# Kernel tuning notes

Measured on AMD Instinct MI355X. Metric: run time of the kernel, lower is better.

## Reference

```python
import jax, jax.numpy as jnp
import numpy as np


def setup_inputs() -> dict:
    key = jax.random.key(0)
    ks = jax.random.split(key, 7)
    B, C, W, H = 4, 256, 128, 128
    s = 1.0 / np.sqrt(C)
    return {
        "x": jax.random.normal(ks[0], (B, C, W, H), dtype=jnp.float32),
        "wq": jax.random.normal(ks[1], (C, C), dtype=jnp.float32) * s,
        "bq": jax.random.normal(ks[2], (C,), dtype=jnp.float32) * s,
        "wk": jax.random.normal(ks[3], (C, C), dtype=jnp.float32) * s,
        "bk": jax.random.normal(ks[4], (C,), dtype=jnp.float32) * s,
        "wv": jax.random.normal(ks[5], (C, C), dtype=jnp.float32) * s,
        "bv": jax.random.normal(ks[6], (C,), dtype=jnp.float32) * s,
    }


def reference(x, wq, bq, wk, bk, wv, bv):
    B, C, W, H = x.shape
    N = W * H
    xf = x.reshape(B, C, N)  # flatten spatial: (B, C, N)
    # 1x1 convs are channel-mixing GEMMs: out[b,o,n] = sum_c w[o,c] x[b,c,n] + b[o]
    q = jnp.einsum('oc,bcn->bon', wq, xf) + bq[:, None]
    k = jnp.einsum('oc,bcn->bon', wk, xf) + bk[:, None]
    v = jnp.einsum('oc,bcn->bon', wv, xf) + bv[:, None]
    # channel-channel energy: (B, C, C)
    energy = jnp.einsum('bcn,bdn->bcd', q, k) / jnp.sqrt(jnp.float32(N))
    attention = jax.nn.softmax(energy, axis=-1)
    out = jnp.einsum('bcd,bdn->bcn', attention, v)
    return out.reshape(B, C, W, H) + x
```

## Files before the change

### kernel.cpp

```cpp
#include <hip/hip_runtime.h>
#include <stdint.h>

#define BB 4
#define CC 256
#define NN 16384
#define NSL 32

typedef unsigned short u16;
typedef __attribute__((ext_vector_type(8))) __bf16 bf16x8;
typedef __attribute__((ext_vector_type(4))) float f32x4;

__device__ __forceinline__ u16 f2bf(float f) {
  union { float f; uint32_t u; } c;
  c.f = f;
  uint32_t u = c.u;
  return (u16)((u + 0x7fffu + ((u >> 16) & 1u)) >> 16);
}

__device__ __forceinline__ void g2l16(const u16* g, u16* l) {
  __builtin_amdgcn_global_load_lds((__attribute__((address_space(1))) void*)g,
                                   (__attribute__((address_space(3))) void*)l, 16, 0, 0);
}

__device__ __forceinline__ void stage256x32_w8(const u16* src, int stride, u16* lds, int tid) {
  int r = tid >> 2;
  int c = (tid & 3) << 3;
  g2l16(src + (size_t)r * stride + c, lds + r * 32 + c);
  g2l16(src + (size_t)(r + 128) * stride + c, lds + (r + 128) * 32 + c);
}

__device__ __forceinline__ void mfma_tile(const u16* As, const u16* Bs, int mb, int nb,
                                          int l16, int q8, f32x4 acc[4][4]) {
  bf16x8 af[4], bf[4];
#pragma unroll
  for (int i = 0; i < 4; i++) af[i] = *(const bf16x8*)&As[(mb + i * 16 + l16) * 32 + q8];
#pragma unroll
  for (int i = 0; i < 4; i++) bf[i] = *(const bf16x8*)&Bs[(nb + i * 16 + l16) * 32 + q8];
#pragma unroll
  for (int i = 0; i < 4; i++)
#pragma unroll
    for (int j = 0; j < 4; j++)
      acc[i][j] = __builtin_amdgcn_mfma_f32_16x16x32_bf16(af[i], bf[j], acc[i][j], 0, 0, 0);
}

__device__ __forceinline__ void mfma_tile48(const u16* As, const u16* Bs, int mb, int nb,
                                            int l16, int q8, f32x4 acc[4][8]) {
  bf16x8 af[4], bf[8];
#pragma unroll
  for (int i = 0; i < 4; i++) af[i] = *(const bf16x8*)&As[(mb + i * 16 + l16) * 32 + q8];
#pragma unroll
  for (int j = 0; j < 8; j++) bf[j] = *(const bf16x8*)&Bs[(nb + j * 16 + l16) * 32 + q8];
#pragma unroll
  for (int i = 0; i < 4; i++)
#pragma unroll
    for (int j = 0; j < 8; j++)
      acc[i][j] = __builtin_amdgcn_mfma_f32_16x16x32_bf16(af[i], bf[j], acc[i][j], 0, 0, 0);
}

__global__ __launch_bounds__(256) void prep_kernel(const float* __restrict__ x,
                                                   u16* __restrict__ xb,
                                                   u16* __restrict__ xbT,
                                                   float* __restrict__ s_part) {
  __shared__ float t[64][65];
  __shared__ float rs[64][4];
  int n0 = blockIdx.x * 64, c0 = blockIdx.y * 64, bz = blockIdx.z;
  int tid = threadIdx.x;
  int rr0 = tid >> 4, q4 = (tid & 15) * 4;
  const float* xs = x + ((size_t)bz * CC + c0) * NN + n0;
  u16* xbp = xb + ((size_t)bz * CC + c0) * NN + n0;
#pragma unroll
  for (int cc = rr0; cc < 64; cc += 16) {
    float4 v = *(const float4*)&xs[(size_t)cc * NN + q4];
    t[cc][q4] = v.x; t[cc][q4 + 1] = v.y; t[cc][q4 + 2] = v.z; t[cc][q4 + 3] = v.w;
    union { u16 h[4]; uint2 u; } pk;
    pk.h[0] = f2bf(v.x); pk.h[1] = f2bf(v.y); pk.h[2] = f2bf(v.z); pk.h[3] = f2bf(v.w);
    *(uint2*)&xbp[(size_t)cc * NN + q4] = pk.u;
  }
  __syncthreads();
  {
    int r = tid >> 2, q = tid & 3;
    float p = 0.f;
#pragma unroll
    for (int i = 0; i < 16; i++) p += t[r][q * 16 + i];
    rs[r][q] = p;
  }
  u16* od = xbT + ((size_t)bz * NN + n0) * CC + c0;
#pragma unroll
  for (int nn = rr0; nn < 64; nn += 16) {
    union { u16 h[4]; uint2 u; } pk;
    pk.h[0] = f2bf(t[q4][nn]); pk.h[1] = f2bf(t[q4 + 1][nn]);
    pk.h[2] = f2bf(t[q4 + 2][nn]); pk.h[3] = f2bf(t[q4 + 3][nn]);
    *(uint2*)&od[(size_t)nn * CC + q4] = pk.u;
  }
  __syncthreads();
  if (tid < 64)
    s_part[((size_t)bz * 256 + blockIdx.x) * CC + c0 + tid] =
        rs[tid][0] + rs[tid][1] + rs[tid][2] + rs[tid][3];
}

__global__ __launch_bounds__(512) void gram_kernel(const u16* __restrict__ xb,
                                                   float* __restrict__ Gp) {
  __shared__ u16 As[2][256 * 32];
  int tid = threadIdx.x;
  int d0 = blockIdx.x * 128;
  int sl = blockIdx.y, bz = blockIdx.z;
  const u16* A = xb + (size_t)bz * CC * NN + sl * 512;
  f32x4 acc[4][4] = {};
  int wave = tid >> 6, lane = tid & 63;
  int mb = (wave & 3) * 64, nb = d0 + (wave >> 2) * 64;
  int quad = lane >> 4, l16 = lane & 15, q8 = quad * 8;
  for (int kk = 0; kk < 512; kk += 64) {
    stage256x32_w8(A + kk, NN, As[0], tid);
    stage256x32_w8(A + kk + 32, NN, As[1], tid);
    __syncthreads();
    mfma_tile(As[0], As[0], mb, nb, l16, q8, acc);
    mfma_tile(As[1], As[1], mb, nb, l16, q8, acc);
    __syncthreads();
  }
  float* gp = Gp + ((size_t)sl * BB + bz) * CC * CC;
#pragma unroll
  for (int i = 0; i < 4; i++)
#pragma unroll
    for (int j = 0; j < 4; j++)
#pragma unroll
      for (int r = 0; r < 4; r++)
        gp[(size_t)(mb + i * 16 + quad * 4 + r) * CC + nb + j * 16 + l16] =
            acc[i][j][r];
}

__global__ __launch_bounds__(256) void reduce_kernel(const float* __restrict__ Gp,
                                                     const float* __restrict__ s_part,
                                                     const float* __restrict__ Wk,
                                                     float* __restrict__ G,
                                                     float* __restrict__ s,
                                                     float* __restrict__ WkT) {
  __shared__ float tw[32][33];
  int t = threadIdx.x, blk = blockIdx.x;
  size_t base = ((size_t)blk * 256 + t) * 4;
  float ax = 0.f, ay = 0.f, az = 0.f, aw = 0.f;
#pragma unroll 8
  for (int sl = 0; sl < NSL; sl++) {
    float4 v = *(const float4*)&Gp[(size_t)sl * (BB * CC * CC) + base];
    ax += v.x; ay += v.y; az += v.z; aw += v.w;
  }
  float4 o; o.x = ax; o.y = ay; o.z = az; o.w = aw;
  *(float4*)&G[base] = o;
  if (blk < BB) {
    float a = 0.f;
#pragma unroll 8
    for (int nt = 0; nt < 256; nt++) a += s_part[((size_t)blk * 256 + nt) * CC + t];
    s[blk * CC + t] = a;
  }
  if (blk < 64) {
    int tr = blk >> 3, tc = blk & 7;
    int r = t >> 5, c = t & 31;
#pragma unroll
    for (int i = 0; i < 4; i++)
      tw[r + i * 8][c] = Wk[(size_t)(tr * 32 + r + i * 8) * CC + tc * 32 + c];
    __syncthreads();
#pragma unroll
    for (int i = 0; i < 4; i++)
      WkT[(size_t)(tc * 32 + r + i * 8) * CC + tr * 32 + c] = tw[c][r + i * 8];
  }
}

__global__ __launch_bounds__(512) void mid_kernel(
    const float* __restrict__ G, const float* __restrict__ s,
    const float* __restrict__ Wq, const float* __restrict__ WkT,
    const float* __restrict__ Wv,
    const float* __restrict__ bq, const float* __restrict__ bk,
    const float* __restrict__ bv,
    u16* __restrict__ Mvb, float* __restrict__ bo) {
  __shared__ float sS[CC];
  __shared__ float wqS[4][CC];
  __shared__ float rS[4][CC];
  __shared__ float attS[4][CC];
  __shared__ float part[4][8][CC];
  __shared__ float redA[4][4], redB[4][4], redC[4][4], redD[4][4];
  int t = threadIdx.x;
  int o0 = blockIdx.x * 4, b = blockIdx.y;
  int wv = t >> 6, ln = t & 63;
  int col = t & 255;
  int row_a = t >> 8, row_b = row_a + 2;
  int c4 = ln << 2;
  int d0 = wv << 5;
  if (t < CC) sS[t] = s[b * CC + t];
  {
    const float* wqsrc = Wq + (size_t)o0 * CC;
    ((float*)wqS)[t] = wqsrc[t];
    ((float*)wqS)[t + 512] = wqsrc[t + 512];
  }
  __syncthreads();
  float pa = wqS[row_a][col] * sS[col];
  float pb = wqS[row_b][col] * sS[col];
#pragma unroll
  for (int d = 32; d > 0; d >>= 1) {
    pa += __shfl_xor(pa, d, 64);
    pb += __shfl_xor(pb, d, 64);
  }
  if (ln == 0) { redA[row_a][wv & 3] = pa; redA[row_b][wv & 3] = pb; }
  __syncthreads();
  float up_a = redA[row_a][0] + redA[row_a][1] + redA[row_a][2] + redA[row_a][3] +
               16384.f * bq[o0 + row_a];
  float up_b = redA[row_b][0] + redA[row_b][1] + redA[row_b][2] + redA[row_b][3] +
               16384.f * bq[o0 + row_b];
  const float* Gb = G + (size_t)b * CC * CC;
  {
    f32x4 va[4] = {};
    const float* gp = Gb + (size_t)d0 * CC + c4;
#pragma unroll 8
    for (int i = 0; i < 32; i++) {
      f32x4 g4 = *(const f32x4*)(gp + (size_t)i * CC);
      float w0 = wqS[0][d0 + i], w1 = wqS[1][d0 + i];
      float w2 = wqS[2][d0 + i], w3 = wqS[3][d0 + i];
      va[0] += g4 * w0; va[1] += g4 * w1; va[2] += g4 * w2; va[3] += g4 * w3;
    }
#pragma unroll
    for (int r = 0; r < 4; r++) *(f32x4*)&part[r][wv][c4] = va[r];
  }
  __syncthreads();
  {
    float r_a = bq[o0 + row_a] * sS[col];
    float r_b = bq[o0 + row_b] * sS[col];
#pragma unroll
    for (int w = 0; w < 8; w++) { r_a += part[row_a][w][col]; r_b += part[row_b][w][col]; }
    rS[row_a][col] = r_a;
    rS[row_b][col] = r_b;
  }
  __syncthreads();
  {
    f32x4 ve[4] = {};
    const float* wkp = WkT + (size_t)d0 * CC + c4;
#pragma unroll 8
    for (int i = 0; i < 32; i++) {
      f32x4 w4 = *(const f32x4*)(wkp + (size_t)i * CC);
      float r0 = rS[0][d0 + i], r1 = rS[1][d0 + i];
      float r2 = rS[2][d0 + i], r3 = rS[3][d0 + i];
      ve[0] += w4 * r0; ve[1] += w4 * r1; ve[2] += w4 * r2; ve[3] += w4 * r3;
    }
#pragma unroll
    for (int r = 0; r < 4; r++) *(f32x4*)&part[r][wv][c4] = ve[r];
  }
  __syncthreads();
  float bkc = bk[col];
  float e_a = up_a * bkc, e_b = up_b * bkc;
#pragma unroll
  for (int w = 0; w < 8; w++) { e_a += part[row_a][w][col]; e_b += part[row_b][w][col]; }
  e_a *= 0.0078125f;
  e_b *= 0.0078125f;
  float m_a = e_a, m_b = e_b;
#pragma unroll
  for (int d = 32; d > 0; d >>= 1) {
    m_a = fmaxf(m_a, __shfl_xor(m_a, d, 64));
    m_b = fmaxf(m_b, __shfl_xor(m_b, d, 64));
  }
  if (ln == 0) { redB[row_a][wv & 3] = m_a; redB[row_b][wv & 3] = m_b; }
  __syncthreads();
  m_a = fmaxf(fmaxf(redB[row_a][0], redB[row_a][1]), fmaxf(redB[row_a][2], redB[row_a][3]));
  m_b = fmaxf(fmaxf(redB[row_b][0], redB[row_b][1]), fmaxf(redB[row_b][2], redB[row_b][3]));
  e_a = __expf(e_a - m_a);
  e_b = __expf(e_b - m_b);
  float s_a = e_a, s_b = e_b;
#pragma unroll
  for (int d = 32; d > 0; d >>= 1) {
    s_a += __shfl_xor(s_a, d, 64);
    s_b += __shfl_xor(s_b, d, 64);
  }
  if (ln == 0) { redC[row_a][wv & 3] = s_a; redC[row_b][wv & 3] = s_b; }
  __syncthreads();
  float inv_a = 1.f / (redC[row_a][0] + redC[row_a][1] + redC[row_a][2] + redC[row_a][3]);
  float inv_b = 1.f / (redC[row_b][0] + redC[row_b][1] + redC[row_b][2] + redC[row_b][3]);
  float at_a = e_a * inv_a, at_b = e_b * inv_b;
  attS[row_a][col] = at_a;
  attS[row_b][col] = at_b;
  float bvc = bv[col];
  float ba = at_a * bvc, bb = at_b * bvc;
#pragma unroll
  for (int d = 32; d > 0; d >>= 1) {
    ba += __shfl_xor(ba, d, 64);
    bb += __shfl_xor(bb, d, 64);
  }
  if (ln == 0) { redD[row_a][wv & 3] = ba; redD[row_b][wv & 3] = bb; }
  __syncthreads();
  if (t < 4) bo[b * CC + o0 + t] = redD[t][0] + redD[t][1] + redD[t][2] + redD[t][3];
  {
    f32x4 vm[4] = {};
    const float* wp = Wv + (size_t)d0 * CC + c4;
#pragma unroll 8
    for (int i = 0; i < 32; i++) {
      f32x4 w4 = *(const f32x4*)(wp + (size_t)i * CC);
      float a0 = attS[0][d0 + i], a1 = attS[1][d0 + i];
      float a2 = attS[2][d0 + i], a3 = attS[3][d0 + i];
      vm[0] += w4 * a0; vm[1] += w4 * a1; vm[2] += w4 * a2; vm[3] += w4 * a3;
    }
#pragma unroll
    for (int r = 0; r < 4; r++) *(f32x4*)&part[r][wv][c4] = vm[r];
  }
  __syncthreads();
  float mv_a = 0.f, mv_b = 0.f;
#pragma unroll
  for (int w = 0; w < 8; w++) { mv_a += part[row_a][w][col]; mv_b += part[row_b][w][col]; }
  Mvb[((size_t)b * CC + o0 + row_a) * CC + col] = f2bf(mv_a);
  Mvb[((size_t)b * CC + o0 + row_b) * CC + col] = f2bf(mv_b);
}

__global__ __launch_bounds__(512) void out_kernel(const u16* __restrict__ Mvb,
                                                  const u16* __restrict__ xbT,
                                                  const float* __restrict__ bo,
                                                  const float* __restrict__ x,
                                                  float* __restrict__ out) {
  __shared__ union {
    struct { u16 As[2][256 * 32]; u16 Bs[2][256 * 32]; } st;
    float scr[8][64][20];
  } sm;
  int tid = threadIdx.x;
  int n0 = blockIdx.x * 256, bz = blockIdx.y;
  const u16* A = Mvb + (size_t)bz * CC * CC;
  const u16* Bt = xbT + ((size_t)bz * NN + n0) * CC;
  f32x4 acc[4][8] = {};
  int wave = tid >> 6, lane = tid & 63;
  int mb = (wave & 3) * 64, nb = (wave >> 2) * 128;
  int quad = lane >> 4, l16 = lane & 15, q8 = quad * 8;
  for (int kk = 0; kk < CC; kk += 64) {
    stage256x32_w8(A + kk, CC, sm.st.As[0], tid);
    stage256x32_w8(A + kk + 32, CC, sm.st.As[1], tid);
    stage256x32_w8(Bt + kk, CC, sm.st.Bs[0], tid);
    stage256x32_w8(Bt + kk + 32, CC, sm.st.Bs[1], tid);
    __syncthreads();
    mfma_tile48(sm.st.As[0], sm.st.Bs[0], mb, nb, l16, q8, acc);
    mfma_tile48(sm.st.As[1], sm.st.Bs[1], mb, nb, l16, q8, acc);
    __syncthreads();
  }
  int l4 = lane >> 2;
  int cgl = lane & 3;
  float bc[4];
#pragma unroll
  for (int kq = 0; kq < 4; kq++) bc[kq] = bo[bz * CC + mb + kq * 16 + l4];
#pragma unroll
  for (int j = 0; j < 8; j++) {
#pragma unroll
    for (int i = 0; i < 4; i++)
#pragma unroll
      for (int r = 0; r < 4; r++)
        sm.scr[wave][i * 16 + quad * 4 + r][l16] = acc[i][j][r];
#pragma unroll
    for (int kq = 0; kq < 4; kq++) {
      int rloc = kq * 16 + l4;
      f32x4 v4 = *(const f32x4*)&sm.scr[wave][rloc][cgl * 4];
      int cg = mb + rloc;
      int ng = n0 + nb + j * 16 + cgl * 4;
      size_t idx = ((size_t)bz * CC + cg) * NN + ng;
      float4 xv = *(const float4*)&x[idx];
      float4 o4;
      o4.x = v4[0] + bc[kq] + xv.x;
      o4.y = v4[1] + bc[kq] + xv.y;
      o4.z = v4[2] + bc[kq] + xv.z;
      o4.w = v4[3] + bc[kq] + xv.w;
      *(float4*)&out[idx] = o4;
    }
  }
}

extern "C" void kernel_launch(void* const* d_in, const int* in_sizes, int n_in,
                              void* d_out, int out_size, void* d_ws, size_t ws_size,
                              hipStream_t stream) {
  (void)in_sizes; (void)n_in; (void)out_size; (void)ws_size;
  const float* x = (const float*)d_in[0];
  const float* wq = (const float*)d_in[1];
  const float* bq = (const float*)d_in[2];
  const float* wk = (const float*)d_in[3];
  const float* bk = (const float*)d_in[4];
  const float* wv = (const float*)d_in[5];
  const float* bv = (const float*)d_in[6];
  float* out = (float*)d_out;

  char* ws = (char*)d_ws;
  u16* xb      = (u16*)(ws + 0);
  u16* xbT     = (u16*)(ws + 33554432);
  float* Gp    = (float*)(ws + 67108864);
  float* G     = (float*)(ws + 100663296);
  float* s_prt = (float*)(ws + 101711872);
  float* s     = (float*)(ws + 102760448);
  u16* Mvb     = (u16*)(ws + 102764544);
  float* bo    = (float*)(ws + 103288832);
  float* WkT   = (float*)(ws + 103292928);

  prep_kernel<<<dim3(NN / 64, CC / 64, BB), 256, 0, stream>>>(x, xb, xbT, s_prt);
  gram_kernel<<<dim3(2, NSL, BB), 512, 0, stream>>>(xb, Gp);
  reduce_kernel<<<256, 256, 0, stream>>>(Gp, s_prt, wk, G, s, WkT);
  mid_kernel<<<dim3(CC / 4, BB), 512, 0, stream>>>(G, s, wq, WkT, wv, bq, bk, bv, Mvb, bo);
  out_kernel<<<dim3(NN / 256, BB), 512, 0, stream>>>(Mvb, xbT, bo, x, out);
}
```

Before: 224.2 us.

## Halve out_kernel N tile and widen prep_kernel tile to 128 columns

The output GEMM kernel now uses a 256x128 tile with 4x4 MFMA accumulators per wave instead of 256x256. This doubles the grid and lowers register and LDS use per block, so more blocks can be resident. The prep kernel processes 128 spatial columns per block instead of 64, which halves the number of partial-sum rows that the reduce kernel must accumulate. The trade-off is that the Mvb tile is re-staged twice as often in out_kernel, and prep uses a larger LDS transpose buffer.

```diff
diff --git a/kernel.cpp b/kernel.cpp
--- a/kernel.cpp
+++ b/kernel.cpp
@@ -5,6 +5,7 @@
 #define CC 256
 #define NN 16384
 #define NSL 32
+#define NT 128
 
 typedef unsigned short u16;
 typedef __attribute__((ext_vector_type(8))) __bf16 bf16x8;
@@ -29,6 +30,12 @@
   g2l16(src + (size_t)(r + 128) * stride + c, lds + (r + 128) * 32 + c);
 }
 
+__device__ __forceinline__ void stage128x32_w8(const u16* src, int stride, u16* lds, int tid) {
+  int r = tid >> 2;
+  int c = (tid & 3) << 3;
+  g2l16(src + (size_t)r * stride + c, lds + r * 32 + c);
+}
+
 __device__ __forceinline__ void mfma_tile(const u16* As, const u16* Bs, int mb, int nb,
                                           int l16, int q8, f32x4 acc[4][4]) {
   bf16x8 af[4], bf[4];
@@ -40,20 +47,6 @@
   for (int i = 0; i < 4; i++)
 #pragma unroll
     for (int j = 0; j < 4; j++)
-      acc[i][j] = __builtin_amdgcn_mfma_f32_16x16x32_bf16(af[i], bf[j], acc[i][j], 0, 0, 0);
-}
-
-__device__ __forceinline__ void mfma_tile48(const u16* As, const u16* Bs, int mb, int nb,
-                                            int l16, int q8, f32x4 acc[4][8]) {
-  bf16x8 af[4], bf[8];
-#pragma unroll
-  for (int i = 0; i < 4; i++) af[i] = *(const bf16x8*)&As[(mb + i * 16 + l16) * 32 + q8];
-#pragma unroll
-  for (int j = 0; j < 8; j++) bf[j] = *(const bf16x8*)&Bs[(nb + j * 16 + l16) * 32 + q8];
-#pragma unroll
-  for (int i = 0; i < 4; i++)
-#pragma unroll
-    for (int j = 0; j < 8; j++)
       acc[i][j] = __builtin_amdgcn_mfma_f32_16x16x32_bf16(af[i], bf[j], acc[i][j], 0, 0, 0);
 }
 
@@ -61,40 +54,42 @@
                                                    u16* __restrict__ xb,
                                                    u16* __restrict__ xbT,
                                                    float* __restrict__ s_part) {
-  __shared__ float t[64][65];
+  __shared__ float t[64][129];
   __shared__ float rs[64][4];
-  int n0 = blockIdx.x * 64, c0 = blockIdx.y * 64, bz = blockIdx.z;
+  int n0 = blockIdx.x * 128, c0 = blockIdx.y * 64, bz = blockIdx.z;
   int tid = threadIdx.x;
-  int rr0 = tid >> 4, q4 = (tid & 15) * 4;
+  int rl = tid >> 5;
+  int ql = (tid & 31) * 4;
   const float* xs = x + ((size_t)bz * CC + c0) * NN + n0;
   u16* xbp = xb + ((size_t)bz * CC + c0) * NN + n0;
 #pragma unroll
-  for (int cc = rr0; cc < 64; cc += 16) {
-    float4 v = *(const float4*)&xs[(size_t)cc * NN + q4];
-    t[cc][q4] = v.x; t[cc][q4 + 1] = v.y; t[cc][q4 + 2] = v.z; t[cc][q4 + 3] = v.w;
+  for (int cc = rl; cc < 64; cc += 8) {
+    float4 v = *(const float4*)&xs[(size_t)cc * NN + ql];
+    t[cc][ql] = v.x; t[cc][ql + 1] = v.y; t[cc][ql + 2] = v.z; t[cc][ql + 3] = v.w;
     union { u16 h[4]; uint2 u; } pk;
     pk.h[0] = f2bf(v.x); pk.h[1] = f2bf(v.y); pk.h[2] = f2bf(v.z); pk.h[3] = f2bf(v.w);
-    *(uint2*)&xbp[(size_t)cc * NN + q4] = pk.u;
+    *(uint2*)&xbp[(size_t)cc * NN + ql] = pk.u;
   }
   __syncthreads();
   {
     int r = tid >> 2, q = tid & 3;
     float p = 0.f;
 #pragma unroll
-    for (int i = 0; i < 16; i++) p += t[r][q * 16 + i];
+    for (int i = 0; i < 32; i++) p += t[r][q * 32 + i];
     rs[r][q] = p;
   }
   u16* od = xbT + ((size_t)bz * NN + n0) * CC + c0;
-#pragma unroll
-  for (int nn = rr0; nn < 64; nn += 16) {
+  int rt = tid >> 4, qt = (tid & 15) * 4;
+#pragma unroll
+  for (int nn = rt; nn < 128; nn += 16) {
     union { u16 h[4]; uint2 u; } pk;
-    pk.h[0] = f2bf(t[q4][nn]); pk.h[1] = f2bf(t[q4 + 1][nn]);
-    pk.h[2] = f2bf(t[q4 + 2][nn]); pk.h[3] = f2bf(t[q4 + 3][nn]);
-    *(uint2*)&od[(size_t)nn * CC + q4] = pk.u;
+    pk.h[0] = f2bf(t[qt][nn]); pk.h[1] = f2bf(t[qt + 1][nn]);
+    pk.h[2] = f2bf(t[qt + 2][nn]); pk.h[3] = f2bf(t[qt + 3][nn]);
+    *(uint2*)&od[(size_t)nn * CC + qt] = pk.u;
   }
   __syncthreads();
   if (tid < 64)
-    s_part[((size_t)bz * 256 + blockIdx.x) * CC + c0 + tid] =
+    s_part[((size_t)bz * NT + blockIdx.x) * CC + c0 + tid] =
         rs[tid][0] + rs[tid][1] + rs[tid][2] + rs[tid][3];
 }
 
@@ -148,7 +143,7 @@
   if (blk < BB) {
     float a = 0.f;
 #pragma unroll 8
-    for (int nt = 0; nt < 256; nt++) a += s_part[((size_t)blk * 256 + nt) * CC + t];
+    for (int nt = 0; nt < NT; nt++) a += s_part[((size_t)blk * NT + nt) * CC + t];
     s[blk * CC + t] = a;
   }
   if (blk < 64) {
@@ -304,31 +299,31 @@
   Mvb[((size_t)b * CC + o0 + row_b) * CC + col] = f2bf(mv_b);
 }
 
-__global__ __launch_bounds__(512) void out_kernel(const u16* __restrict__ Mvb,
-                                                  const u16* __restrict__ xbT,
-                                                  const float* __restrict__ bo,
-                                                  const float* __restrict__ x,
-                                                  float* __restrict__ out) {
+__global__ __launch_bounds__(512, 4) void out_kernel(const u16* __restrict__ Mvb,
+                                                     const u16* __restrict__ xbT,
+                                                     const float* __restrict__ bo,
+                                                     const float* __restrict__ x,
+                                                     float* __restrict__ out) {
   __shared__ union {
-    struct { u16 As[2][256 * 32]; u16 Bs[2][256 * 32]; } st;
+    struct { u16 As[2][256 * 32]; u16 Bs[2][128 * 32]; } st;
     float scr[8][64][20];
   } sm;
   int tid = threadIdx.x;
-  int n0 = blockIdx.x * 256, bz = blockIdx.y;
+  int n0 = blockIdx.x * 128, bz = blockIdx.y;
   const u16* A = Mvb + (size_t)bz * CC * CC;
   const u16* Bt = xbT + ((size_t)bz * NN + n0) * CC;
-  f32x4 acc[4][8] = {};
+  f32x4 acc[4][4] = {};
   int wave = tid >> 6, lane = tid & 63;
-  int mb = (wave & 3) * 64, nb = (wave >> 2) * 128;
+  int mb = (wave & 3) * 64, nb = (wave >> 2) * 64;
   int quad = lane >> 4, l16 = lane & 15, q8 = quad * 8;
   for (int kk = 0; kk < CC; kk += 64) {
     stage256x32_w8(A + kk, CC, sm.st.As[0], tid);
     stage256x32_w8(A + kk + 32, CC, sm.st.As[1], tid);
-    stage256x32_w8(Bt + kk, CC, sm.st.Bs[0], tid);
-    stage256x32_w8(Bt + kk + 32, CC, sm.st.Bs[1], tid);
-    __syncthreads();
-    mfma_tile48(sm.st.As[0], sm.st.Bs[0], mb, nb, l16, q8, acc);
-    mfma_tile48(sm.st.As[1], sm.st.Bs[1], mb, nb, l16, q8, acc);
+    stage128x32_w8(Bt + kk, CC, sm.st.Bs[0], tid);
+    stage128x32_w8(Bt + kk + 32, CC, sm.st.Bs[1], tid);
+    __syncthreads();
+    mfma_tile(sm.st.As[0], sm.st.Bs[0], mb, nb, l16, q8, acc);
+    mfma_tile(sm.st.As[1], sm.st.Bs[1], mb, nb, l16, q8, acc);
     __syncthreads();
   }
   int l4 = lane >> 2;
@@ -337,7 +332,7 @@
 #pragma unroll
   for (int kq = 0; kq < 4; kq++) bc[kq] = bo[bz * CC + mb + kq * 16 + l4];
 #pragma unroll
-  for (int j = 0; j < 8; j++) {
+  for (int j = 0; j < 4; j++) {
 #pragma unroll
     for (int i = 0; i < 4; i++)
 #pragma unroll
@@ -385,9 +380,9 @@
   float* bo    = (float*)(ws + 103288832);
   float* WkT   = (float*)(ws + 103292928);
 
-  prep_kernel<<<dim3(NN / 64, CC / 64, BB), 256, 0, stream>>>(x, xb, xbT, s_prt);
+  prep_kernel<<<dim3(NN / 128, CC / 64, BB), 256, 0, stream>>>(x, xb, xbT, s_prt);
   gram_kernel<<<dim3(2, NSL, BB), 512, 0, stream>>>(xb, Gp);
   reduce_kernel<<<256, 256, 0, stream>>>(Gp, s_prt, wk, G, s, WkT);
   mid_kernel<<<dim3(CC / 4, BB), 512, 0, stream>>>(G, s, wq, WkT, wv, bq, bk, bv, Mvb, bo);
-  out_kernel<<<dim3(NN / 256, BB), 512, 0, stream>>>(Mvb, xbT, bo, x, out);
-}
+  out_kernel<<<dim3(NN / 128, BB), 512, 0, stream>>>(Mvb, xbT, bo, x, out);
+}
```

Measured after the change: 207.2 us. 7.6% less time.
